# Kernel optimization log

Hardware: AMD Instinct MI355X
Metric: run time of the kernel (lower is better)

## Reference

```python
import jax, jax.numpy as jnp
import numpy as np

B, F, H, L, K = 16384, 1024, 1024, 256, 7

def _lin(key, fi, fo, lead=()):
    k1, k2 = jax.random.split(key)
    s = 1.0 / np.sqrt(fi)
    W = jax.random.uniform(k1, lead + (fi, fo), jnp.float32, -s, s)
    b = jax.random.uniform(k2, lead + (fo,), jnp.float32, -s, s)
    return W, b

def setup_inputs() -> dict:
    ks = jax.random.split(jax.random.key(0), 16)
    x = jax.random.normal(ks[0], (B, F), jnp.float32)
    t = jax.random.randint(ks[1], (B,), 0, K, jnp.int32)
    y = jax.random.normal(ks[2], (B,), jnp.float32)
    d = jax.random.normal(ks[3], (B,), jnp.float32)
    tw0, tb0 = _lin(ks[4], F, L)
    tw1, tb1 = _lin(ks[5], L, L)
    tw2, tb2 = _lin(ks[6], L, K)
    yw0, yb0 = _lin(ks[7], F, H)
    yw1, yb1 = _lin(ks[8], H, H)
    yhW, yhb = _lin(ks[9], H, 2, (K,))
    dw0, db0 = _lin(ks[10], F, H)
    dw1, db1 = _lin(ks[11], H, H)
    dhW, dhb = _lin(ks[12], H, 2, (K,))
    zw0, zb0 = _lin(ks[13], F + 2, H)
    zw1, zb1 = _lin(ks[14], H, H)
    zhW, zhb = _lin(ks[15], H, 2 * L, (K,))
    return dict(x=x, t=t, y=y, d=d, tw0=tw0, tb0=tb0, tw1=tw1, tb1=tb1, tw2=tw2, tb2=tb2,
                yw0=yw0, yb0=yb0, yw1=yw1, yb1=yb1, yhW=yhW, yhb=yhb,
                dw0=dw0, db0=db0, dw1=dw1, db1=db1, dhW=dhW, dhb=dhb,
                zw0=zw0, zb0=zb0, zw1=zw1, zb1=zb1, zhW=zhW, zhb=zhb)

def _mlp2(x, w0, b0, w1, b1):
    # FullyConnected([in, H, H], final_activation=ELU)
    return jax.nn.elu(jax.nn.elu(x @ w0 + b0) @ w1 + b1)

def _select(hidden, t, hW, hb):
    # dense compute of all K treatment heads, then per-row gather by t
    all_out = jnp.einsum('bh,khd->bkd', hidden, hW) + hb  # [B, K, D]
    return jnp.take_along_axis(all_out, t[:, None, None], axis=1)[:, 0]

def _normal_head(sel):
    # pyro NormalNet head on a scalar outcome
    loc = jnp.clip(sel[:, 0:1], -1e6, 1e6)
    scale = jnp.minimum(jax.nn.softplus(sel[:, 1:2]) + 1e-3, 1e6)
    return loc, scale

def _diagnormal_head(sel):
    loc = jnp.clip(sel[:, :L], -100.0, 100.0)
    scale = jnp.minimum(jax.nn.softplus(sel[:, L:]) + 0.001, 100.0)
    return loc, scale

def reference(x, t, y, d, tw0, tb0, tw1, tb1, tw2, tb2,
              yw0, yb0, yw1, yb1, yhW, yhb,
              dw0, db0, dw1, db1, dhW, dhb,
              zw0, zb0, zw1, zb1, zhW, zhb):
    # t_nn: MultinormNet, ELU final activation then clamp(-10, 10)
    t_logits = jnp.clip(jax.nn.elu(_mlp2(x, tw0, tb0, tw1, tb1) @ tw2 + tb2), -10.0, 10.0)
    # y_dist(t, x)
    hy = _mlp2(x, yw0, yb0, yw1, yb1)
    y_loc, y_scale = _normal_head(_select(hy, t, yhW, yhb))
    # d_dist(t, x)
    hd = _mlp2(x, dw0, db0, dw1, db1)
    d_loc, d_scale = _normal_head(_select(hd, t, dhW, dhb))
    # z_dist(y, d, t, x): hidden from cat([y, d, x])
    hz = _mlp2(jnp.concatenate([y[:, None], d[:, None], x], axis=-1), zw0, zb0, zw1, zb1)
    z_loc, z_scale = _diagnormal_head(_select(hz, t, zhW, zhb))
    # [B, K + 4 + 2L]
    return jnp.concatenate([t_logits, y_loc, y_scale, d_loc, d_scale, z_loc, z_scale], axis=-1)
```

## Files before the change

### kernel.cpp

```cpp
#include <hip/hip_runtime.h>
#include <hip/hip_bf16.h>
#include <cstdint>
#include <cstddef>

typedef __hip_bfloat16 bf16;
typedef __bf16 bf16x8 __attribute__((ext_vector_type(8)));
typedef float f32x4 __attribute__((ext_vector_type(4)));

#define DEVFN static __device__ __forceinline__

DEVFN void async16(const void* g, void* l) {
  __builtin_amdgcn_global_load_lds(
      (const __attribute__((address_space(1))) uint32_t*)g,
      (__attribute__((address_space(3))) uint32_t*)l, 16, 0, 0);
}

DEVFN float eluf(float v) { return v > 0.f ? v : expm1f(v); }
DEVFN float softplusf(float x) {
  return x > 0.f ? x + log1pf(expf(-x)) : log1pf(expf(x));
}

DEVFN void kloop(const bf16* gA0, const bf16* gA1, const bf16* gB0,
                 const bf16* gB1, bf16* lA0, bf16* lA1, bf16* lB0, bf16* lB1,
                 const bf16* aBase, const bf16* bBase, f32x4 (&acc)[4][4],
                 int kiters) {
  for (int kt = 0; kt < kiters; ++kt) {
    async16(gA0, lA0); async16(gA1, lA1);
    async16(gB0, lB0); async16(gB1, lB1);
    gA0 += 32; gA1 += 32; gB0 += 32; gB1 += 32;
    __syncthreads();
    bf16x8 af[4], bfv[4];
#pragma unroll
    for (int r = 0; r < 4; ++r) af[r] = *(const bf16x8*)(aBase + r * 512);
#pragma unroll
    for (int c = 0; c < 4; ++c) bfv[c] = *(const bf16x8*)(bBase + c * 512);
#pragma unroll
    for (int r = 0; r < 4; ++r)
#pragma unroll
      for (int c = 0; c < 4; ++c)
        acc[r][c] = __builtin_amdgcn_mfma_f32_16x16x32_bf16(af[r], bfv[c], acc[r][c], 0, 0, 0);
    __syncthreads();
  }
}

DEVFN void transpose_tile(const float* src, bf16* dst, int R, int C, int bx, int by) {
  __shared__ float tile[32][33];
  const int c0 = bx * 32, r0 = by * 32;
  const int tx = threadIdx.x & 31, ty = threadIdx.x >> 5;
#pragma unroll
  for (int rr = ty; rr < 32; rr += 8)
    tile[rr][tx] = src[(size_t)(r0 + rr) * C + c0 + tx];
  __syncthreads();
#pragma unroll
  for (int rr = ty; rr < 32; rr += 8)
    dst[(size_t)(c0 + rr) * R + r0 + tx] = __float2bfloat16(tile[tx][rr]);
}

__global__ __launch_bounds__(256) void prep_all_k(
    const float* __restrict__ x, bf16* __restrict__ xb,
    const float* __restrict__ yw0, const float* __restrict__ dw0,
    const float* __restrict__ zw0, const float* __restrict__ tw0,
    bf16* __restrict__ BtL1,
    const float* __restrict__ yw1, const float* __restrict__ dw1,
    const float* __restrict__ zw1, bf16* __restrict__ BtL2,
    const float* __restrict__ tw1, bf16* __restrict__ tw1t,
    const float* __restrict__ zhW, bf16* __restrict__ zhWt,
    const float* __restrict__ yb0, const float* __restrict__ db0,
    const float* __restrict__ zb0, const float* __restrict__ tb0,
    const float* __restrict__ yb1, const float* __restrict__ db1,
    const float* __restrict__ zb1,
    float* __restrict__ biasAll, float* __restrict__ r0All,
    float* __restrict__ r1All, float* __restrict__ biasL2) {
  int l = blockIdx.x;
  if (l < 8192) {
    size_t i = ((size_t)l * 256 + threadIdx.x) * 8;
    float4 v0 = *(const float4*)(x + i);
    float4 v1 = *(const float4*)(x + i + 4);
    union { bf16 h[8]; uint4 u; } o;
    o.h[0] = __float2bfloat16(v0.x); o.h[1] = __float2bfloat16(v0.y);
    o.h[2] = __float2bfloat16(v0.z); o.h[3] = __float2bfloat16(v0.w);
    o.h[4] = __float2bfloat16(v1.x); o.h[5] = __float2bfloat16(v1.y);
    o.h[6] = __float2bfloat16(v1.z); o.h[7] = __float2bfloat16(v1.w);
    *(uint4*)(xb + i) = o.u;
    return;
  }
  l -= 8192;
  if (l < 4096) {
    int z = l >> 10, rem = l & 1023, bx = rem & 31, by = rem >> 5;
    const float* src = (z == 0) ? yw0 : (z == 1) ? dw0 : (z == 2) ? zw0 + 2048 : tw0;
    int C = (z == 3) ? 256 : 1024;
    if (bx * 32 < C)
      transpose_tile(src, BtL1 + (size_t)z * 1024 * 1024, 1024, C, bx, by);
    return;
  }
  l -= 4096;
  if (l < 3072) {
    int z = l >> 10, rem = l & 1023, bx = rem & 31, by = rem >> 5;
    const float* src = (z == 0) ? yw1 : (z == 1) ? dw1 : zw1;
    transpose_tile(src, BtL2 + (size_t)z * 1024 * 1024, 1024, 1024, bx, by);
    return;
  }
  l -= 3072;
  if (l < 64) {
    transpose_tile(tw1, tw1t, 256, 256, l & 7, l >> 3);
    return;
  }
  l -= 64;
  if (l < 3584) {
    int z = l >> 9, rem = l & 511, bx = rem & 15, by = rem >> 4;
    transpose_tile(zhW + (size_t)z * 1024 * 512, zhWt + (size_t)z * 512 * 1024,
                   1024, 512, bx, by);
    return;
  }
  l -= 3584;
  {
    int i = l * 256 + threadIdx.x;
    if (i >= 3328) return;
    float b;
    if (i < 1024) b = yb0[i];
    else if (i < 2048) b = db0[i - 1024];
    else if (i < 3072) b = zb0[i - 2048];
    else b = tb0[i - 3072];
    biasAll[i] = b;
    bool inz = (i >= 2048 && i < 3072);
    r0All[i] = inz ? zw0[i - 2048] : 0.f;
    r1All[i] = inz ? zw0[1024 + (i - 2048)] : 0.f;
    if (i < 3072)
      biasL2[i] = (i < 1024) ? yb1[i] : (i < 2048) ? db1[i - 1024] : zb1[i - 2048];
  }
}

__global__ __launch_bounds__(256) void bucketize_k(const int* __restrict__ t,
                                                   int* __restrict__ cnt,
                                                   int* __restrict__ pos) {
  int b = blockIdx.x * 256 + threadIdx.x;
  pos[b] = atomicAdd(&cnt[t[b]], 1);
}
__global__ void segk(const int* __restrict__ cnt, int* __restrict__ seg) {
  if (threadIdx.x == 0) {
    int s = 0;
    for (int k = 0; k < 7; ++k) { seg[k] = s; s += cnt[k]; }
    seg[7] = s;
  }
}
__global__ __launch_bounds__(256) void rankk(const int* __restrict__ t,
                                             const int* __restrict__ pos,
                                             const int* __restrict__ seg,
                                             int* __restrict__ rank,
                                             int* __restrict__ sids) {
  int b = blockIdx.x * 256 + threadIdx.x;
  int r = seg[t[b]] + pos[b];
  rank[b] = r;
  sids[r] = b;
}

__global__ __launch_bounds__(256) void gemm_l1_k(
    const bf16* __restrict__ A, const bf16* __restrict__ Bt,
    const float* __restrict__ biasAll, const float* __restrict__ r0All,
    const float* __restrict__ r1All, const float* __restrict__ yv,
    const float* __restrict__ dv, bf16* __restrict__ a1y,
    bf16* __restrict__ a1d, bf16* __restrict__ a1z, bf16* __restrict__ ht1) {
  __shared__ bf16 As[128 * 32];
  __shared__ bf16 Bs[128 * 32];
  const int tid = threadIdx.x, lane = tid & 63, wid = tid >> 6;
  const int wm = wid >> 1, wn = wid & 1, quad = lane >> 4, l15 = lane & 15;
  const int id = blockIdx.x;
  const int xcd = id & 7, lid = id >> 3;
  const int pass = lid / 208, rem = lid - pass * 208;
  const int mt = xcd * 16 + pass * 8 + (rem & 7), nt = rem >> 3;
  const int bm0 = mt * 128, bn0 = nt * 128;
  const int sr = tid >> 2, sc = (tid & 3) * 8;
  f32x4 acc[4][4] = {};
  kloop(A + (size_t)(bm0 + sr) * 1024 + sc,
        A + (size_t)(bm0 + 64 + sr) * 1024 + sc,
        Bt + (size_t)(bn0 + sr) * 1024 + sc,
        Bt + (size_t)(bn0 + 64 + sr) * 1024 + sc,
        &As[tid * 8], &As[2048 + tid * 8], &Bs[tid * 8], &Bs[2048 + tid * 8],
        &As[(wm * 64 + l15) * 32 + quad * 8],
        &Bs[(wn * 64 + l15) * 32 + quad * 8], acc, 32);
  const int g = nt >> 3;
  bf16* dst = (g == 0) ? a1y : (g == 1) ? a1d : (g == 2) ? a1z : ht1;
  const int ldc = (g == 3) ? 256 : 1024;
  const int colb = bn0 - g * 1024;
  float bv[4], z0[4], z1[4];
#pragma unroll
  for (int c = 0; c < 4; ++c) {
    int gn = bn0 + wn * 64 + c * 16 + l15;
    bv[c] = biasAll[gn]; z0[c] = r0All[gn]; z1[c] = r1All[gn];
  }
#pragma unroll
  for (int r = 0; r < 4; ++r) {
#pragma unroll
    for (int q = 0; q < 4; ++q) {
      int gm = bm0 + wm * 64 + r * 16 + quad * 4 + q;
      float yy = yv[gm], dd = dv[gm];
#pragma unroll
      for (int c = 0; c < 4; ++c) {
        float v = acc[r][c][q] + bv[c] + yy * z0[c] + dd * z1[c];
        dst[(size_t)gm * ldc + colb + wn * 64 + c * 16 + l15] = __float2bfloat16(eluf(v));
      }
    }
  }
}

__global__ __launch_bounds__(256) void gemm_l2t_k(
    const bf16* __restrict__ a1y, const bf16* __restrict__ a1d,
    const bf16* __restrict__ a1z, const bf16* __restrict__ ht1,
    const bf16* __restrict__ BtL2, const bf16* __restrict__ tw1t,
    const float* __restrict__ biasL2, const float* __restrict__ tb1,
    bf16* __restrict__ hyd, bf16* __restrict__ hzg, bf16* __restrict__ ht2,
    const int* __restrict__ rank) {
  __shared__ bf16 As[128 * 32];
  __shared__ bf16 Bs[128 * 32];
  const int tid = threadIdx.x, lane = tid & 63, wid = tid >> 6;
  const int wm = wid >> 1, wn = wid & 1, quad = lane >> 4, l15 = lane & 15;
  const int id = blockIdx.x;
  int bm0, bn0, Ka, g;
  const bf16 *Aptr, *Bptr;
  if (id < 3072) {
    const int xcd = id & 7, lid = id >> 3;
    const int pass = lid / 192, rem = lid - pass * 192;
    const int mt = xcd * 16 + pass * 8 + (rem & 7), nt = rem >> 3;
    bm0 = mt * 128; bn0 = nt * 128; Ka = 1024;
    g = nt >> 3;
    Aptr = (g == 0) ? a1y : (g == 1) ? a1d : a1z;
    Bptr = BtL2;
  } else {
    const int local = id - 3072;
    bm0 = (local >> 1) * 128; bn0 = (local & 1) * 128; Ka = 256;
    g = 3; Aptr = ht1; Bptr = tw1t;
  }
  const int sr = tid >> 2, sc = (tid & 3) * 8;
  f32x4 acc[4][4] = {};
  kloop(Aptr + (size_t)(bm0 + sr) * Ka + sc,
        Aptr + (size_t)(bm0 + 64 + sr) * Ka + sc,
        Bptr + (size_t)(bn0 + sr) * Ka + sc,
        Bptr + (size_t)(bn0 + 64 + sr) * Ka + sc,
        &As[tid * 8], &As[2048 + tid * 8], &Bs[tid * 8], &Bs[2048 + tid * 8],
        &As[(wm * 64 + l15) * 32 + quad * 8],
        &Bs[(wn * 64 + l15) * 32 + quad * 8], acc, Ka >> 5);
  const float* bias = (g == 3) ? tb1 : biasL2;
  float bv[4];
#pragma unroll
  for (int c = 0; c < 4; ++c) bv[c] = bias[bn0 + wn * 64 + c * 16 + l15];
#pragma unroll
  for (int r = 0; r < 4; ++r) {
#pragma unroll
    for (int q = 0; q < 4; ++q) {
      int gm = bm0 + wm * 64 + r * 16 + quad * 4 + q;
      bf16* dst; size_t rowoff;
      if (g == 2) { dst = hzg; rowoff = (size_t)rank[gm] * 1024 + (size_t)(bn0 - 2048); }
      else if (g == 3) { dst = ht2; rowoff = (size_t)gm * 256 + bn0; }
      else { dst = hyd; rowoff = (size_t)gm * 2048 + bn0; }
#pragma unroll
      for (int c = 0; c < 4; ++c) {
        float v = acc[r][c][q] + bv[c];
        dst[rowoff + wn * 64 + c * 16 + l15] = __float2bfloat16(eluf(v));
      }
    }
  }
}

__global__ __launch_bounds__(256) void zhead_k(
    const bf16* __restrict__ hzg, const bf16* __restrict__ zhWt,
    const float* __restrict__ zhb, const int* __restrict__ seg,
    const int* __restrict__ cnts, const int* __restrict__ sids,
    float* __restrict__ out) {
  const int kb = blockIdx.z;
  const int cnt = cnts[kb];
  const int bm0 = blockIdx.y * 128;
  if (bm0 >= cnt) return;
  __shared__ bf16 As[128 * 32];
  __shared__ bf16 Bs[64 * 32];
  const int tid = threadIdx.x, lane = tid & 63, wid = tid >> 6;
  const int wm = wid >> 1, wn = wid & 1, quad = lane >> 4, l15 = lane & 15;
  const int n0 = blockIdx.x * 64;
  const int base = seg[kb];
  const int sr = tid >> 2, sc = (tid & 3) * 8;
  int r0i = bm0 + sr;      if (r0i >= cnt) r0i = cnt - 1;
  int r1i = bm0 + 64 + sr; if (r1i >= cnt) r1i = cnt - 1;
  const bf16* gA0 = hzg + (size_t)(base + r0i) * 1024 + sc;
  const bf16* gA1 = hzg + (size_t)(base + r1i) * 1024 + sc;
  const bf16* gB0 = zhWt + (size_t)kb * 512 * 1024 + (size_t)(n0 + sr) * 1024 + sc;
  bf16 *lA0 = &As[tid * 8], *lA1 = &As[2048 + tid * 8], *lB0 = &Bs[tid * 8];
  const bf16* aBase = &As[(wm * 64 + l15) * 32 + quad * 8];
  const bf16* bBase = &Bs[(wn * 32 + l15) * 32 + quad * 8];
  f32x4 acc[4][2] = {};
  for (int kt = 0; kt < 32; ++kt) {
    async16(gA0, lA0); async16(gA1, lA1); async16(gB0, lB0);
    gA0 += 32; gA1 += 32; gB0 += 32;
    __syncthreads();
    bf16x8 af[4], bfv[2];
#pragma unroll
    for (int r = 0; r < 4; ++r) af[r] = *(const bf16x8*)(aBase + r * 512);
#pragma unroll
    for (int c = 0; c < 2; ++c) bfv[c] = *(const bf16x8*)(bBase + c * 512);
#pragma unroll
    for (int r = 0; r < 4; ++r)
#pragma unroll
      for (int c = 0; c < 2; ++c)
        acc[r][c] = __builtin_amdgcn_mfma_f32_16x16x32_bf16(af[r], bfv[c], acc[r][c], 0, 0, 0);
    __syncthreads();
  }
  const float* bias = zhb + (size_t)kb * 512;
  float bv[2]; int gnn[2];
#pragma unroll
  for (int c = 0; c < 2; ++c) {
    gnn[c] = n0 + wn * 32 + c * 16 + l15;
    bv[c] = bias[gnn[c]];
  }
#pragma unroll
  for (int r = 0; r < 4; ++r)
#pragma unroll
    for (int q = 0; q < 4; ++q) {
      int lm = bm0 + wm * 64 + r * 16 + quad * 4 + q;
      if (lm < cnt) {
        int gm = sids[base + lm];
        size_t ob = (size_t)gm * 523 + 11;
#pragma unroll
        for (int c = 0; c < 2; ++c) {
          float v = acc[r][c][q] + bv[c];
          int n = gnn[c];
          out[ob + n] = (n < 256) ? fminf(fmaxf(v, -100.f), 100.f)
                                  : fminf(softplusf(v) + 0.001f, 100.f);
        }
      }
    }
}

__global__ __launch_bounds__(256) void heads_k(
    const bf16* __restrict__ hyd, const bf16* __restrict__ ht2,
    const int* __restrict__ t, const float* __restrict__ yhW,
    const float* __restrict__ yhb, const float* __restrict__ dhW,
    const float* __restrict__ dhb, const float* __restrict__ tw2,
    const float* __restrict__ tb2, float* __restrict__ out) {
  const int wv = threadIdx.x >> 6, lane = threadIdx.x & 63;
  if (blockIdx.x < 4096) {
    const int b = blockIdx.x * 4 + wv;
    const int tb = t[b];
    const float* yW = yhW + (size_t)tb * 2048;
    const float* dW = dhW + (size_t)tb * 2048;
    float s0 = 0.f, s1 = 0.f, s2 = 0.f, s3 = 0.f;
    for (int i = lane; i < 1024; i += 64) {
      float a = __bfloat162float(hyd[(size_t)b * 2048 + i]);
      float c = __bfloat162float(hyd[(size_t)b * 2048 + 1024 + i]);
      s0 += a * yW[2 * i]; s1 += a * yW[2 * i + 1];
      s2 += c * dW[2 * i]; s3 += c * dW[2 * i + 1];
    }
#pragma unroll
    for (int off = 32; off > 0; off >>= 1) {
      s0 += __shfl_down(s0, off); s1 += __shfl_down(s1, off);
      s2 += __shfl_down(s2, off); s3 += __shfl_down(s3, off);
    }
    if (lane == 0) {
      size_t o = (size_t)b * 523;
      out[o + 7] = fminf(fmaxf(s0 + yhb[tb * 2], -1e6f), 1e6f);
      out[o + 8] = fminf(softplusf(s1 + yhb[tb * 2 + 1]) + 1e-3f, 1e6f);
      out[o + 9] = fminf(fmaxf(s2 + dhb[tb * 2], -1e6f), 1e6f);
      out[o + 10] = fminf(softplusf(s3 + dhb[tb * 2 + 1]) + 1e-3f, 1e6f);
    }
  } else {
    const int b = (blockIdx.x - 4096) * 4 + wv;
    float h[4];
#pragma unroll
    for (int j = 0; j < 4; ++j)
      h[j] = __bfloat162float(ht2[(size_t)b * 256 + lane * 4 + j]);
    float pp[7];
#pragma unroll
    for (int kk = 0; kk < 7; ++kk) {
      float s = 0.f;
#pragma unroll
      for (int j = 0; j < 4; ++j) s += h[j] * tw2[(lane * 4 + j) * 7 + kk];
      pp[kk] = s;
    }
#pragma unroll
    for (int kk = 0; kk < 7; ++kk)
#pragma unroll
      for (int off = 32; off > 0; off >>= 1) pp[kk] += __shfl_down(pp[kk], off);
    if (lane == 0) {
#pragma unroll
      for (int kk = 0; kk < 7; ++kk) {
        float v = eluf(pp[kk] + tb2[kk]);
        out[(size_t)b * 523 + kk] = fminf(fmaxf(v, -10.f), 10.f);
      }
    }
  }
}

extern "C" void kernel_launch(void* const* d_in, const int* in_sizes, int n_in,
                              void* d_out, int out_size, void* d_ws, size_t ws_size,
                              hipStream_t stream) {
  const float* x   = (const float*)d_in[0];
  const int*   t   = (const int*)d_in[1];
  const float* yv  = (const float*)d_in[2];
  const float* dv  = (const float*)d_in[3];
  const float* tw0 = (const float*)d_in[4];
  const float* tb0 = (const float*)d_in[5];
  const float* tw1 = (const float*)d_in[6];
  const float* tb1 = (const float*)d_in[7];
  const float* tw2 = (const float*)d_in[8];
  const float* tb2 = (const float*)d_in[9];
  const float* yw0 = (const float*)d_in[10];
  const float* yb0 = (const float*)d_in[11];
  const float* yw1 = (const float*)d_in[12];
  const float* yb1 = (const float*)d_in[13];
  const float* yhW = (const float*)d_in[14];
  const float* yhb = (const float*)d_in[15];
  const float* dw0 = (const float*)d_in[16];
  const float* db0 = (const float*)d_in[17];
  const float* dw1 = (const float*)d_in[18];
  const float* db1 = (const float*)d_in[19];
  const float* dhW = (const float*)d_in[20];
  const float* dhb = (const float*)d_in[21];
  const float* zw0 = (const float*)d_in[22];
  const float* zb0 = (const float*)d_in[23];
  const float* zw1 = (const float*)d_in[24];
  const float* zb1 = (const float*)d_in[25];
  const float* zhW = (const float*)d_in[26];
  const float* zhb = (const float*)d_in[27];
  float* out = (float*)d_out;

  const int B = 16384;
  char* p = (char*)d_ws;
  auto take = [&](size_t bytes) {
    char* r = p;
    p += (bytes + 255) & ~(size_t)255;
    return r;
  };
  bf16*  BtL1    = (bf16*)take((size_t)3328 * 1024 * 2);
  bf16*  BtL2    = (bf16*)take((size_t)3072 * 1024 * 2);
  bf16*  tw1t    = (bf16*)take((size_t)256 * 256 * 2);
  bf16*  zhWt    = (bf16*)take((size_t)7 * 512 * 1024 * 2);
  float* biasAll = (float*)take(3328 * 4);
  float* r0All   = (float*)take(3328 * 4);
  float* r1All   = (float*)take(3328 * 4);
  float* biasL2  = (float*)take(3072 * 4);
  int*   cnt     = (int*)take(8 * 4);
  int*   seg     = (int*)take(8 * 4);
  int*   pos     = (int*)take((size_t)B * 4);
  int*   rank    = (int*)take((size_t)B * 4);
  int*   sids    = (int*)take((size_t)B * 4);
  bf16*  xb      = (bf16*)take((size_t)B * 1024 * 2);
  bf16*  a1y     = (bf16*)take((size_t)B * 1024 * 2);
  bf16*  a1d     = (bf16*)take((size_t)B * 1024 * 2);
  bf16*  a1z     = (bf16*)take((size_t)B * 1024 * 2);
  bf16*  ht1     = (bf16*)take((size_t)B * 256 * 2);
  bf16*  hyd     = (bf16*)take((size_t)B * 2048 * 2);
  bf16*  ht2     = (bf16*)take((size_t)B * 256 * 2);
  bf16*  hzg     = xb;

  hipMemsetAsync(cnt, 0, 8 * 4, stream);
  bucketize_k<<<B / 256, 256, 0, stream>>>(t, cnt, pos);
  segk<<<1, 64, 0, stream>>>(cnt, seg);
  rankk<<<B / 256, 256, 0, stream>>>(t, pos, seg, rank, sids);
  prep_all_k<<<19021, 256, 0, stream>>>(x, xb, yw0, dw0, zw0, tw0, BtL1,
                                        yw1, dw1, zw1, BtL2, tw1, tw1t, zhW, zhWt,
                                        yb0, db0, zb0, tb0, yb1, db1, zb1,
                                        biasAll, r0All, r1All, biasL2);
  gemm_l1_k<<<3328, 256, 0, stream>>>(xb, BtL1, biasAll, r0All, r1All,
                                      yv, dv, a1y, a1d, a1z, ht1);
  gemm_l2t_k<<<3328, 256, 0, stream>>>(a1y, a1d, a1z, ht1, BtL2, tw1t,
                                       biasL2, tb1, hyd, hzg, ht2, rank);
  zhead_k<<<dim3(8, 24, 7), 256, 0, stream>>>(hzg, zhWt, zhb, seg, cnt, sids, out);
  heads_k<<<8192, 256, 0, stream>>>(hyd, ht2, t, yhW, yhb, dhW, dhb, tw2, tb2, out);
}
```

Baseline: 733.6 us.

## Use BK=64 XOR-swizzled GEMM tiles, fuse bucketing and tail kernels

The GEMM main loop now stages 64-wide K slices instead of 32, with an XOR swizzle on LDS columns. This halves the number of barrier pairs per tile and aims to avoid LDS bank conflicts, at the cost of doubling shared memory per block. The three bucketing kernels plus the memset are replaced by a single 1024-thread block that computes counts, segments and ranks in one pass. The z-head GEMM and the y/d/t head kernel are merged into one launch, removing launch gaps and the tail of the earlier kernel.

Measured after the change: 703.0 us. 4.2% less time.

```diff
diff --git a/kernel.cpp b/kernel.cpp
--- a/kernel.cpp
+++ b/kernel.cpp
@@ -20,25 +20,35 @@
   return x > 0.f ? x + log1pf(expf(-x)) : log1pf(expf(x));
 }
 
-DEVFN void kloop(const bf16* gA0, const bf16* gA1, const bf16* gB0,
-                 const bf16* gB1, bf16* lA0, bf16* lA1, bf16* lB0, bf16* lB1,
-                 const bf16* aBase, const bf16* bBase, f32x4 (&acc)[4][4],
-                 int kiters) {
+template <int NCHB, int NFB>
+DEVFN void kloop64(const bf16* (&gA)[4], const bf16* (&gB)[NCHB], bf16* As,
+                   bf16* Bs, int tid, const bf16* aBase, const bf16* bBase,
+                   const int (&colsel)[2], f32x4 (&acc)[4][NFB], int kiters) {
   for (int kt = 0; kt < kiters; ++kt) {
-    async16(gA0, lA0); async16(gA1, lA1);
-    async16(gB0, lB0); async16(gB1, lB1);
-    gA0 += 32; gA1 += 32; gB0 += 32; gB1 += 32;
+#pragma unroll
+    for (int c = 0; c < 4; ++c) async16(gA[c], As + c * 2048 + tid * 8);
+#pragma unroll
+    for (int c = 0; c < NCHB; ++c) async16(gB[c], Bs + c * 2048 + tid * 8);
+#pragma unroll
+    for (int c = 0; c < 4; ++c) gA[c] += 64;
+#pragma unroll
+    for (int c = 0; c < NCHB; ++c) gB[c] += 64;
     __syncthreads();
-    bf16x8 af[4], bfv[4];
-#pragma unroll
-    for (int r = 0; r < 4; ++r) af[r] = *(const bf16x8*)(aBase + r * 512);
-#pragma unroll
-    for (int c = 0; c < 4; ++c) bfv[c] = *(const bf16x8*)(bBase + c * 512);
-#pragma unroll
-    for (int r = 0; r < 4; ++r)
-#pragma unroll
-      for (int c = 0; c < 4; ++c)
-        acc[r][c] = __builtin_amdgcn_mfma_f32_16x16x32_bf16(af[r], bfv[c], acc[r][c], 0, 0, 0);
+#pragma unroll
+    for (int s = 0; s < 2; ++s) {
+      bf16x8 af[4], bfv[NFB];
+#pragma unroll
+      for (int r = 0; r < 4; ++r)
+        af[r] = *(const bf16x8*)(aBase + r * 1024 + colsel[s]);
+#pragma unroll
+      for (int c = 0; c < NFB; ++c)
+        bfv[c] = *(const bf16x8*)(bBase + c * 1024 + colsel[s]);
+#pragma unroll
+      for (int r = 0; r < 4; ++r)
+#pragma unroll
+        for (int c = 0; c < NFB; ++c)
+          acc[r][c] = __builtin_amdgcn_mfma_f32_16x16x32_bf16(af[r], bfv[c], acc[r][c], 0, 0, 0);
+    }
     __syncthreads();
   }
 }
@@ -130,28 +140,41 @@
   }
 }
 
-__global__ __launch_bounds__(256) void bucketize_k(const int* __restrict__ t,
-                                                   int* __restrict__ cnt,
-                                                   int* __restrict__ pos) {
-  int b = blockIdx.x * 256 + threadIdx.x;
-  pos[b] = atomicAdd(&cnt[t[b]], 1);
-}
-__global__ void segk(const int* __restrict__ cnt, int* __restrict__ seg) {
-  if (threadIdx.x == 0) {
+__global__ __launch_bounds__(1024) void book_k(const int* __restrict__ t,
+                                               int* __restrict__ cnt,
+                                               int* __restrict__ seg,
+                                               int* __restrict__ rank,
+                                               int* __restrict__ sids) {
+  __shared__ int h[8], sseg[8];
+  const int tid = threadIdx.x;
+  if (tid < 8) h[tid] = 0;
+  __syncthreads();
+  int tv[16], lc[7] = {0, 0, 0, 0, 0, 0, 0};
+  const int base = tid * 16;
+#pragma unroll
+  for (int i = 0; i < 16; ++i) { tv[i] = t[base + i]; lc[tv[i]]++; }
+  int myoff[7];
+#pragma unroll
+  for (int k = 0; k < 7; ++k) myoff[k] = atomicAdd(&h[k], lc[k]);
+  __syncthreads();
+  if (tid == 0) {
     int s = 0;
-    for (int k = 0; k < 7; ++k) { seg[k] = s; s += cnt[k]; }
-    seg[7] = s;
-  }
-}
-__global__ __launch_bounds__(256) void rankk(const int* __restrict__ t,
-                                             const int* __restrict__ pos,
-                                             const int* __restrict__ seg,
-                                             int* __restrict__ rank,
-                                             int* __restrict__ sids) {
-  int b = blockIdx.x * 256 + threadIdx.x;
-  int r = seg[t[b]] + pos[b];
-  rank[b] = r;
-  sids[r] = b;
+    for (int k = 0; k < 7; ++k) { sseg[k] = s; s += h[k]; }
+    sseg[7] = s;
+  }
+  __syncthreads();
+  if (tid < 7) { cnt[tid] = h[tid]; seg[tid] = sseg[tid]; }
+  if (tid == 7) seg[7] = sseg[7];
+  int cur[7];
+#pragma unroll
+  for (int k = 0; k < 7; ++k) cur[k] = sseg[k] + myoff[k];
+#pragma unroll
+  for (int i = 0; i < 16; ++i) {
+    int b = base + i, k = tv[i];
+    int r = cur[k]++;
+    rank[b] = r;
+    sids[r] = b;
+  }
 }
 
 __global__ __launch_bounds__(256) void gemm_l1_k(
@@ -160,8 +183,8 @@
     const float* __restrict__ r1All, const float* __restrict__ yv,
     const float* __restrict__ dv, bf16* __restrict__ a1y,
     bf16* __restrict__ a1d, bf16* __restrict__ a1z, bf16* __restrict__ ht1) {
-  __shared__ bf16 As[128 * 32];
-  __shared__ bf16 Bs[128 * 32];
+  __shared__ bf16 As[128 * 64];
+  __shared__ bf16 Bs[128 * 64];
   const int tid = threadIdx.x, lane = tid & 63, wid = tid >> 6;
   const int wm = wid >> 1, wn = wid & 1, quad = lane >> 4, l15 = lane & 15;
   const int id = blockIdx.x;
@@ -169,15 +192,22 @@
   const int pass = lid / 208, rem = lid - pass * 208;
   const int mt = xcd * 16 + pass * 8 + (rem & 7), nt = rem >> 3;
   const int bm0 = mt * 128, bn0 = nt * 128;
-  const int sr = tid >> 2, sc = (tid & 3) * 8;
+  const int sr3 = tid >> 3, scol = ((tid & 7) ^ (sr3 & 7)) * 8;
+  const bf16* gA[4];
+  const bf16* gB[4];
+#pragma unroll
+  for (int c = 0; c < 4; ++c) {
+    gA[c] = A + (size_t)(bm0 + c * 32 + sr3) * 1024 + scol;
+    gB[c] = Bt + (size_t)(bn0 + c * 32 + sr3) * 1024 + scol;
+  }
+  const bf16* aBase = &As[(wm * 64 + l15) * 64];
+  const bf16* bBase = &Bs[(wn * 64 + l15) * 64];
+  int colsel[2];
+#pragma unroll
+  for (int s = 0; s < 2; ++s) colsel[s] = ((s * 4 + quad) ^ (l15 & 7)) * 8;
   f32x4 acc[4][4] = {};
-  kloop(A + (size_t)(bm0 + sr) * 1024 + sc,
-        A + (size_t)(bm0 + 64 + sr) * 1024 + sc,
-        Bt + (size_t)(bn0 + sr) * 1024 + sc,
-        Bt + (size_t)(bn0 + 64 + sr) * 1024 + sc,
-        &As[tid * 8], &As[2048 + tid * 8], &Bs[tid * 8], &Bs[2048 + tid * 8],
-        &As[(wm * 64 + l15) * 32 + quad * 8],
-        &Bs[(wn * 64 + l15) * 32 + quad * 8], acc, 32);
+  kloop64<4, 4>(gA, gB, As, Bs, tid, aBase, bBase, colsel, acc, 16);
+
   const int g = nt >> 3;
   bf16* dst = (g == 0) ? a1y : (g == 1) ? a1d : (g == 2) ? a1z : ht1;
   const int ldc = (g == 3) ? 256 : 1024;
@@ -210,8 +240,8 @@
     const float* __restrict__ biasL2, const float* __restrict__ tb1,
     bf16* __restrict__ hyd, bf16* __restrict__ hzg, bf16* __restrict__ ht2,
     const int* __restrict__ rank) {
-  __shared__ bf16 As[128 * 32];
-  __shared__ bf16 Bs[128 * 32];
+  __shared__ bf16 As[128 * 64];
+  __shared__ bf16 Bs[128 * 64];
   const int tid = threadIdx.x, lane = tid & 63, wid = tid >> 6;
   const int wm = wid >> 1, wn = wid & 1, quad = lane >> 4, l15 = lane & 15;
   const int id = blockIdx.x;
@@ -230,15 +260,22 @@
     bm0 = (local >> 1) * 128; bn0 = (local & 1) * 128; Ka = 256;
     g = 3; Aptr = ht1; Bptr = tw1t;
   }
-  const int sr = tid >> 2, sc = (tid & 3) * 8;
+  const int sr3 = tid >> 3, scol = ((tid & 7) ^ (sr3 & 7)) * 8;
+  const bf16* gA[4];
+  const bf16* gB[4];
+#pragma unroll
+  for (int c = 0; c < 4; ++c) {
+    gA[c] = Aptr + (size_t)(bm0 + c * 32 + sr3) * Ka + scol;
+    gB[c] = Bptr + (size_t)(bn0 + c * 32 + sr3) * Ka + scol;
+  }
+  const bf16* aBase = &As[(wm * 64 + l15) * 64];
+  const bf16* bBase = &Bs[(wn * 64 + l15) * 64];
+  int colsel[2];
+#pragma unroll
+  for (int s = 0; s < 2; ++s) colsel[s] = ((s * 4 + quad) ^ (l15 & 7)) * 8;
   f32x4 acc[4][4] = {};
-  kloop(Aptr + (size_t)(bm0 + sr) * Ka + sc,
-        Aptr + (size_t)(bm0 + 64 + sr) * Ka + sc,
-        Bptr + (size_t)(bn0 + sr) * Ka + sc,
-        Bptr + (size_t)(bn0 + 64 + sr) * Ka + sc,
-        &As[tid * 8], &As[2048 + tid * 8], &Bs[tid * 8], &Bs[2048 + tid * 8],
-        &As[(wm * 64 + l15) * 32 + quad * 8],
-        &Bs[(wn * 64 + l15) * 32 + quad * 8], acc, Ka >> 5);
+  kloop64<4, 4>(gA, gB, As, Bs, tid, aBase, bBase, colsel, acc, Ka >> 6);
+
   const float* bias = (g == 3) ? tb1 : biasL2;
   float bv[4];
 #pragma unroll
@@ -261,82 +298,78 @@
   }
 }
 
-__global__ __launch_bounds__(256) void zhead_k(
+#define ZMT 28
+#define ZB (7 * ZMT * 8)
+__global__ __launch_bounds__(256) void tail_k(
     const bf16* __restrict__ hzg, const bf16* __restrict__ zhWt,
     const float* __restrict__ zhb, const int* __restrict__ seg,
     const int* __restrict__ cnts, const int* __restrict__ sids,
-    float* __restrict__ out) {
-  const int kb = blockIdx.z;
-  const int cnt = cnts[kb];
-  const int bm0 = blockIdx.y * 128;
-  if (bm0 >= cnt) return;
-  __shared__ bf16 As[128 * 32];
-  __shared__ bf16 Bs[64 * 32];
-  const int tid = threadIdx.x, lane = tid & 63, wid = tid >> 6;
-  const int wm = wid >> 1, wn = wid & 1, quad = lane >> 4, l15 = lane & 15;
-  const int n0 = blockIdx.x * 64;
-  const int base = seg[kb];
-  const int sr = tid >> 2, sc = (tid & 3) * 8;
-  int r0i = bm0 + sr;      if (r0i >= cnt) r0i = cnt - 1;
-  int r1i = bm0 + 64 + sr; if (r1i >= cnt) r1i = cnt - 1;
-  const bf16* gA0 = hzg + (size_t)(base + r0i) * 1024 + sc;
-  const bf16* gA1 = hzg + (size_t)(base + r1i) * 1024 + sc;
-  const bf16* gB0 = zhWt + (size_t)kb * 512 * 1024 + (size_t)(n0 + sr) * 1024 + sc;
-  bf16 *lA0 = &As[tid * 8], *lA1 = &As[2048 + tid * 8], *lB0 = &Bs[tid * 8];
-  const bf16* aBase = &As[(wm * 64 + l15) * 32 + quad * 8];
-  const bf16* bBase = &Bs[(wn * 32 + l15) * 32 + quad * 8];
-  f32x4 acc[4][2] = {};
-  for (int kt = 0; kt < 32; ++kt) {
-    async16(gA0, lA0); async16(gA1, lA1); async16(gB0, lB0);
-    gA0 += 32; gA1 += 32; gB0 += 32;
-    __syncthreads();
-    bf16x8 af[4], bfv[2];
-#pragma unroll
-    for (int r = 0; r < 4; ++r) af[r] = *(const bf16x8*)(aBase + r * 512);
-#pragma unroll
-    for (int c = 0; c < 2; ++c) bfv[c] = *(const bf16x8*)(bBase + c * 512);
-#pragma unroll
-    for (int r = 0; r < 4; ++r)
-#pragma unroll
-      for (int c = 0; c < 2; ++c)
-        acc[r][c] = __builtin_amdgcn_mfma_f32_16x16x32_bf16(af[r], bfv[c], acc[r][c], 0, 0, 0);
-    __syncthreads();
-  }
-  const float* bias = zhb + (size_t)kb * 512;
-  float bv[2]; int gnn[2];
-#pragma unroll
-  for (int c = 0; c < 2; ++c) {
-    gnn[c] = n0 + wn * 32 + c * 16 + l15;
-    bv[c] = bias[gnn[c]];
-  }
-#pragma unroll
-  for (int r = 0; r < 4; ++r)
-#pragma unroll
-    for (int q = 0; q < 4; ++q) {
-      int lm = bm0 + wm * 64 + r * 16 + quad * 4 + q;
-      if (lm < cnt) {
-        int gm = sids[base + lm];
-        size_t ob = (size_t)gm * 523 + 11;
-#pragma unroll
-        for (int c = 0; c < 2; ++c) {
-          float v = acc[r][c][q] + bv[c];
-          int n = gnn[c];
-          out[ob + n] = (n < 256) ? fminf(fmaxf(v, -100.f), 100.f)
-                                  : fminf(softplusf(v) + 0.001f, 100.f);
-        }
-      }
-    }
-}
-
-__global__ __launch_bounds__(256) void heads_k(
     const bf16* __restrict__ hyd, const bf16* __restrict__ ht2,
     const int* __restrict__ t, const float* __restrict__ yhW,
     const float* __restrict__ yhb, const float* __restrict__ dhW,
     const float* __restrict__ dhb, const float* __restrict__ tw2,
     const float* __restrict__ tb2, float* __restrict__ out) {
-  const int wv = threadIdx.x >> 6, lane = threadIdx.x & 63;
-  if (blockIdx.x < 4096) {
-    const int b = blockIdx.x * 4 + wv;
+  __shared__ bf16 As[128 * 64];
+  __shared__ bf16 Bs[64 * 64];
+  const int tid = threadIdx.x, lane = tid & 63, wid = tid >> 6;
+  const int wv = wid, quad = lane >> 4, l15 = lane & 15;
+  if (blockIdx.x < ZB) {
+    const int kb = blockIdx.x / (ZMT * 8);
+    const int r = blockIdx.x % (ZMT * 8);
+    const int cnt = cnts[kb];
+    const int bm0 = (r >> 3) * 128;
+    if (bm0 >= cnt) return;
+    const int n0 = (r & 7) * 64;
+    const int wm = wid >> 1, wn = wid & 1;
+    const int base = seg[kb];
+    const int sr3 = tid >> 3, scol = ((tid & 7) ^ (sr3 & 7)) * 8;
+    const bf16* gA[4];
+    const bf16* gB[2];
+#pragma unroll
+    for (int c = 0; c < 4; ++c) {
+      int rr = bm0 + c * 32 + sr3;
+      if (rr >= cnt) rr = cnt - 1;
+      gA[c] = hzg + (size_t)(base + rr) * 1024 + scol;
+    }
+#pragma unroll
+    for (int c = 0; c < 2; ++c)
+      gB[c] = zhWt + (size_t)kb * 512 * 1024 + (size_t)(n0 + c * 32 + sr3) * 1024 + scol;
+    const bf16* aBase = &As[(wm * 64 + l15) * 64];
+    const bf16* bBase = &Bs[(wn * 32 + l15) * 64];
+    int colsel[2];
+#pragma unroll
+    for (int s = 0; s < 2; ++s) colsel[s] = ((s * 4 + quad) ^ (l15 & 7)) * 8;
+    f32x4 acc[4][2] = {};
+    kloop64<2, 2>(gA, gB, As, Bs, tid, aBase, bBase, colsel, acc, 16);
+    const float* bias = zhb + (size_t)kb * 512;
+    float bv[2]; int gnn[2];
+#pragma unroll
+    for (int c = 0; c < 2; ++c) {
+      gnn[c] = n0 + wn * 32 + c * 16 + l15;
+      bv[c] = bias[gnn[c]];
+    }
+#pragma unroll
+    for (int r2 = 0; r2 < 4; ++r2)
+#pragma unroll
+      for (int q = 0; q < 4; ++q) {
+        int lm = bm0 + wm * 64 + r2 * 16 + quad * 4 + q;
+        if (lm < cnt) {
+          int gm = sids[base + lm];
+          size_t ob = (size_t)gm * 523 + 11;
+#pragma unroll
+          for (int c = 0; c < 2; ++c) {
+            float v = acc[r2][c][q] + bv[c];
+            int n = gnn[c];
+            out[ob + n] = (n < 256) ? fminf(fmaxf(v, -100.f), 100.f)
+                                    : fminf(softplusf(v) + 0.001f, 100.f);
+          }
+        }
+      }
+    return;
+  }
+  const int hid = blockIdx.x - ZB;
+  if (hid < 4096) {
+    const int b = hid * 4 + wv;
     const int tb = t[b];
     const float* yW = yhW + (size_t)tb * 2048;
     const float* dW = dhW + (size_t)tb * 2048;
@@ -360,7 +393,7 @@
       out[o + 10] = fminf(softplusf(s3 + dhb[tb * 2 + 1]) + 1e-3f, 1e6f);
     }
   } else {
-    const int b = (blockIdx.x - 4096) * 4 + wv;
+    const int b = (hid - 4096) * 4 + wv;
     float h[4];
 #pragma unroll
     for (int j = 0; j < 4; ++j)
@@ -437,7 +470,6 @@
   float* biasL2  = (float*)take(3072 * 4);
   int*   cnt     = (int*)take(8 * 4);
   int*   seg     = (int*)take(8 * 4);
-  int*   pos     = (int*)take((size_t)B * 4);
   int*   rank    = (int*)take((size_t)B * 4);
   int*   sids    = (int*)take((size_t)B * 4);
   bf16*  xb      = (bf16*)take((size_t)B * 1024 * 2);
@@ -449,10 +481,7 @@
   bf16*  ht2     = (bf16*)take((size_t)B * 256 * 2);
   bf16*  hzg     = xb;
 
-  hipMemsetAsync(cnt, 0, 8 * 4, stream);
-  bucketize_k<<<B / 256, 256, 0, stream>>>(t, cnt, pos);
-  segk<<<1, 64, 0, stream>>>(cnt, seg);
-  rankk<<<B / 256, 256, 0, stream>>>(t, pos, seg, rank, sids);
+  book_k<<<1, 1024, 0, stream>>>(t, cnt, seg, rank, sids);
   prep_all_k<<<19021, 256, 0, stream>>>(x, xb, yw0, dw0, zw0, tw0, BtL1,
                                         yw1, dw1, zw1, BtL2, tw1, tw1t, zhW, zhWt,
                                         yb0, db0, zb0, tb0, yb1, db1, zb1,
@@ -461,6 +490,7 @@
                                       yv, dv, a1y, a1d, a1z, ht1);
   gemm_l2t_k<<<3328, 256, 0, stream>>>(a1y, a1d, a1z, ht1, BtL2, tw1t,
                                        biasL2, tb1, hyd, hzg, ht2, rank);
-  zhead_k<<<dim3(8, 24, 7), 256, 0, stream>>>(hzg, zhWt, zhb, seg, cnt, sids, out);
-  heads_k<<<8192, 256, 0, stream>>>(hyd, ht2, t, yhW, yhb, dhW, dhb, tw2, tb2, out);
-}
+  tail_k<<<ZB + 8192, 256, 0, stream>>>(hzg, zhWt, zhb, seg, cnt, sids,
+                                        hyd, ht2, t, yhW, yhb, dhW, dhb,
+                                        tw2, tb2, out);
+}
```
